# Kernel optimization log

Measured on AMD Instinct MI355X. Metric: run time of the kernel, lower is better.

## Reference

```python
import math
import jax, jax.numpy as jnp
import numpy as np

D = 2048
NH = 16
HD = D // NH
B_IMG = 32
H_ORIG, W_ORIG = 28, 36
POOL = 2
HF, WF = H_ORIG // POOL, W_ORIG // POOL  # 14, 18
T = HF * WF                              # 252 tokens per image
S_TOTAL = B_IMG * T                      # 8064
EPS = 1e-6


def setup_inputs() -> dict:
    key = jax.random.key(0)
    ks = jax.random.split(key, 12)
    w = lambda k, shp: jax.random.normal(k, shp, dtype=jnp.float32) * 0.02
    return {
        'semantic_hidden': jax.random.normal(ks[0], (1, S_TOTAL, D), jnp.float32),
        'vggt_features': jax.random.normal(ks[1], (1, S_TOTAL, D), jnp.float32),
        'grid_thw': jnp.tile(jnp.array([[1, H_ORIG, W_ORIG]], dtype=jnp.int64), (B_IMG, 1)),
        'ln1_w': jnp.ones((D,), jnp.float32), 'ln1_b': jnp.zeros((D,), jnp.float32),
        'ln2_w': jnp.ones((D,), jnp.float32), 'ln2_b': jnp.zeros((D,), jnp.float32),
        'Wq': w(ks[2], (D, D)), 'Wk': w(ks[3], (D, D)),
        'Wv': w(ks[4], (D, D)), 'Wo': w(ks[5], (D, D)),
        'imp_w1': w(ks[6], (D // 4, D)), 'imp_b1': jnp.zeros((D // 4,), jnp.float32),
        'imp_w2': w(ks[7], (1, D // 4)), 'imp_b2': jnp.zeros((1,), jnp.float32),
        'gate_w': w(ks[8], (NH // 2, D)), 'gate_b': jnp.zeros((NH // 2,), jnp.float32),
        'gate': jnp.asarray(0.5, jnp.float32),  # torch init is 0.0 (output would be all-zero); use 0.5 for a meaningful baseline
    }


def _layernorm(x, w, b):
    mu = jnp.mean(x, axis=-1, keepdims=True)
    var = jnp.var(x, axis=-1, keepdims=True)
    return (x - mu) * jax.lax.rsqrt(var + EPS) * w + b


def _spatial_bias(h_feat, w_feat, dtype):
    y = jnp.arange(h_feat, dtype=dtype)
    x = jnp.arange(w_feat, dtype=dtype)
    gy, gx = jnp.meshgrid(y, x, indexing='ij')
    coords = jnp.stack([gy.reshape(-1), gx.reshape(-1)], axis=-1)  # [N, 2]
    diff = coords[:, None, :] - coords[None, :, :]
    dist = jnp.sqrt(jnp.sum(diff * diff, axis=-1))  # [N, N]
    diag_len = math.sqrt(h_feat ** 2 + w_feat ** 2) + 1e-6
    return -dist / diag_len


def reference(semantic_hidden, vggt_features, grid_thw, ln1_w, ln1_b, ln2_w, ln2_b,
              Wq, Wk, Wv, Wo, imp_w1, imp_b1, imp_w2, imp_b2, gate_w, gate_b, gate):
    sem = _layernorm(semantic_hidden, ln1_w, ln1_b)
    vgg = _layernorm(vggt_features, ln2_w, ln2_b)
    B_orig, S_total, Dm = sem.shape

    # grid_thw is a static host constant -> Python ints (shapes must be static)
    h_feat = int(np.asarray(grid_thw)[0, 1]) // POOL
    w_feat = int(np.asarray(grid_thw)[0, 2]) // POOL
    tokens = h_feat * w_feat
    num_images = S_total // tokens

    q_in = sem.reshape(num_images, tokens, Dm)   # [B, S, D]
    kv_in = vgg.reshape(num_images, tokens, Dm)
    B, S = num_images, tokens

    q = (q_in @ Wq.T).reshape(B, S, NH, HD).transpose(0, 2, 1, 3)   # [B, H, S, hd]
    k = (kv_in @ Wk.T).reshape(B, S, NH, HD).transpose(0, 2, 1, 3)
    v = (kv_in @ Wv.T).reshape(B, S, NH, HD).transpose(0, 2, 1, 3)

    attn = jnp.einsum('bhqd,bhkd->bhqk', q, k) / math.sqrt(HD)       # [B, H, S, S]

    # spatial bias on first half of heads, gated per (image, query)
    sp_bias = _spatial_bias(h_feat, w_feat, q.dtype)                 # [S, S]
    gate_score = jax.nn.sigmoid(q_in @ gate_w.T + gate_b)            # [B, S, H/2]
    gate_score = gate_score.transpose(0, 2, 1)[..., None]            # [B, H/2, S, 1]
    split = NH // 2
    attn = attn.at[:, :split].add(sp_bias[None, None] * gate_score)

    # importance gate: log-importance bias over keys, shared across heads
    hidden = jax.nn.relu(q_in @ imp_w1.T + imp_b1)
    importance = jax.nn.sigmoid(hidden @ imp_w2.T + imp_b2)          # [B, S, 1]
    attn = attn + jnp.log(importance + 0.1).reshape(B, 1, 1, S)

    probs = jax.nn.softmax(attn, axis=-1)
    out = jnp.einsum('bhqk,bhkd->bhqd', probs, v)                    # [B, H, S, hd]
    out = out.transpose(0, 2, 1, 3).reshape(B, S, Dm)
    out = out.reshape(B_orig, S_total, Dm) @ Wo.T
    return jnp.tanh(gate) * out
```

## Files before the change

### kernel.cpp

```cpp
#include <hip/hip_runtime.h>
#include <hip/hip_bf16.h>
#include <math.h>

typedef __bf16 bf16_t;
typedef __bf16 bf16x8 __attribute__((ext_vector_type(8)));
typedef float f32x4v __attribute__((ext_vector_type(4)));
typedef unsigned short ushort_t;

#define SL_TOTAL 8064
#define DMODEL 2048
#define NHEAD 16
#define HDIM 128
#define SEQ 252

__device__ __forceinline__ bf16_t f2bf(float f) {
  unsigned u = __builtin_bit_cast(unsigned, f);
  u += 0x7fffu + ((u >> 16) & 1u);
  ushort_t h = (ushort_t)(u >> 16);
  return __builtin_bit_cast(bf16_t, h);
}
__device__ __forceinline__ float bf2f(bf16_t b) {
  unsigned u = ((unsigned)__builtin_bit_cast(ushort_t, b)) << 16;
  return __builtin_bit_cast(float, u);
}

__global__ __launch_bounds__(256) void cvt_kernel(const float* __restrict__ src,
                                                  bf16_t* __restrict__ dst, int n) {
  int i = (blockIdx.x * 256 + threadIdx.x) * 8;
  if (i >= n) return;
  float4 a = *(const float4*)(src + i);
  float4 b = *(const float4*)(src + i + 4);
  bf16x8 o;
  o[0] = f2bf(a.x); o[1] = f2bf(a.y); o[2] = f2bf(a.z); o[3] = f2bf(a.w);
  o[4] = f2bf(b.x); o[5] = f2bf(b.y); o[6] = f2bf(b.z); o[7] = f2bf(b.w);
  *(bf16x8*)(dst + i) = o;
}

__global__ __launch_bounds__(256) void ln_kernel(
    const float* __restrict__ sem, const float* __restrict__ vgg,
    const float* __restrict__ w1, const float* __restrict__ b1,
    const float* __restrict__ w2, const float* __restrict__ b2,
    bf16_t* __restrict__ o1, bf16_t* __restrict__ o2) {
  const float* x; const float* w; const float* bb; bf16_t* o;
  int row = blockIdx.x;
  if (blockIdx.y == 0) { x = sem; w = w1; bb = b1; o = o1; }
  else                 { x = vgg; w = w2; bb = b2; o = o2; }
  x += (size_t)row * DMODEL; o += (size_t)row * DMODEL;
  int t = threadIdx.x, wid = t >> 6, lane = t & 63;
  float4 va = *(const float4*)(x + t * 8);
  float4 vb = *(const float4*)(x + t * 8 + 4);
  float s  = va.x + va.y + va.z + va.w + vb.x + vb.y + vb.z + vb.w;
  float ss = va.x*va.x + va.y*va.y + va.z*va.z + va.w*va.w
           + vb.x*vb.x + vb.y*vb.y + vb.z*vb.z + vb.w*vb.w;
  #pragma unroll
  for (int m = 1; m < 64; m <<= 1) { s += __shfl_xor(s, m); ss += __shfl_xor(ss, m); }
  __shared__ float rs[4], rss[4];
  if (lane == 0) { rs[wid] = s; rss[wid] = ss; }
  __syncthreads();
  float st = rs[0] + rs[1] + rs[2] + rs[3];
  float sst = rss[0] + rss[1] + rss[2] + rss[3];
  float mu = st * (1.0f / 2048.0f);
  float var = sst * (1.0f / 2048.0f) - mu * mu;
  float rstd = rsqrtf(var + 1e-6f);
  float4 wa = *(const float4*)(w + t * 8);
  float4 wb = *(const float4*)(w + t * 8 + 4);
  float4 ba = *(const float4*)(bb + t * 8);
  float4 bb4 = *(const float4*)(bb + t * 8 + 4);
  bf16x8 ov;
  ov[0] = f2bf((va.x - mu) * rstd * wa.x + ba.x);
  ov[1] = f2bf((va.y - mu) * rstd * wa.y + ba.y);
  ov[2] = f2bf((va.z - mu) * rstd * wa.z + ba.z);
  ov[3] = f2bf((va.w - mu) * rstd * wa.w + ba.w);
  ov[4] = f2bf((vb.x - mu) * rstd * wb.x + bb4.x);
  ov[5] = f2bf((vb.y - mu) * rstd * wb.y + bb4.y);
  ov[6] = f2bf((vb.z - mu) * rstd * wb.z + bb4.z);
  ov[7] = f2bf((vb.w - mu) * rstd * wb.w + bb4.w);
  *(bf16x8*)(o + t * 8) = ov;
}

template <int EPI>
__global__ __launch_bounds__(256, 2) void gemm_bt(
    const bf16_t* __restrict__ A, const bf16_t* __restrict__ B,
    void* __restrict__ C, void* __restrict__ C2,
    const float* __restrict__ bias, const float* __restrict__ gatep,
    int M, int N, int K, int nnt) {
  __shared__ bf16_t As[2][128 * 64];
  __shared__ bf16_t Bs[2][128 * 64];
  const int nblk = gridDim.x;
  const int orig = blockIdx.x;
  const int qd = nblk >> 3, rr = nblk & 7, xc = orig & 7, lin = orig >> 3;
  const int wg = (xc < rr ? xc * (qd + 1) : rr * (qd + 1) + (xc - rr) * qd) + lin;
  const int mtile = wg / nnt;
  const int ntile = wg - mtile * nnt;
  const int m0 = mtile * 128, n0 = ntile * 128;

  const int tid = threadIdx.x;
  const int wid = tid >> 6, lane = tid & 63;
  const int l15 = lane & 15, l4 = lane >> 4;
  const int wm = (wid >> 1) * 64, wn = (wid & 1) * 64;
  const int srow = lane >> 3;
  const int scol = 8 * ((lane & 7) ^ (lane >> 3));

  f32x4v acc[4][4] = {};
  const int nkt = K >> 6;

  auto stage = [&](int kt, int buf) {
    const int k0 = kt << 6;
    #pragma unroll
    for (int it = 0; it < 4; ++it) {
      int chunk = wid + 4 * it;
      int row = chunk * 8 + srow;
      const bf16_t* ga = A + (size_t)(m0 + row) * K + k0 + scol;
      const bf16_t* gb = B + (size_t)(n0 + row) * K + k0 + scol;
      bf16_t* la = &As[buf][chunk * 512];
      bf16_t* lb = &Bs[buf][chunk * 512];
      __builtin_amdgcn_global_load_lds((const __attribute__((address_space(1))) unsigned int*)ga,
                                       (__attribute__((address_space(3))) unsigned int*)la, 16, 0, 0);
      __builtin_amdgcn_global_load_lds((const __attribute__((address_space(1))) unsigned int*)gb,
                                       (__attribute__((address_space(3))) unsigned int*)lb, 16, 0, 0);
    }
  };

  stage(0, 0);
  for (int kt = 0; kt < nkt; ++kt) {
    int buf = kt & 1;
    __syncthreads();
    if (kt + 1 < nkt) stage(kt + 1, buf ^ 1);
    const char* as = (const char*)As[buf];
    const char* bs = (const char*)Bs[buf];
    #pragma unroll
    for (int ki = 0; ki < 2; ++ki) {
      int cb = ki * 64 + l4 * 16;
      bf16x8 af[4], bfv[4];
      #pragma unroll
      for (int mi = 0; mi < 4; ++mi) {
        int row = wm + mi * 16 + l15;
        af[mi] = *(const bf16x8*)(as + row * 128 + (cb ^ ((row & 7) << 4)));
      }
      #pragma unroll
      for (int ni = 0; ni < 4; ++ni) {
        int row = wn + ni * 16 + l15;
        bfv[ni] = *(const bf16x8*)(bs + row * 128 + (cb ^ ((row & 7) << 4)));
      }
      #pragma unroll
      for (int mi = 0; mi < 4; ++mi)
        #pragma unroll
        for (int ni = 0; ni < 4; ++ni)
          acc[mi][ni] = __builtin_amdgcn_mfma_f32_16x16x32_bf16(af[mi], bfv[ni], acc[mi][ni], 0, 0, 0);
    }
    __syncthreads();
  }

  float scale = 1.0f;
  if (EPI == 2) scale = tanhf(gatep[0]);
  bf16_t* Cb = (bf16_t*)C;
  int colbase = n0;
  int ldc = N;
  if (EPI == 3) {
    ldc = 2048;
    if (n0 >= 2048) { Cb = (bf16_t*)C2; colbase = n0 - 2048; }
  }
  #pragma unroll
  for (int mi = 0; mi < 4; ++mi) {
    #pragma unroll
    for (int ni = 0; ni < 4; ++ni) {
      int c = colbase + wn + ni * 16 + l15;
      #pragma unroll
      for (int j = 0; j < 4; ++j) {
        int r = m0 + wm + mi * 16 + 4 * l4 + j;
        float v = acc[mi][ni][j];
        if (EPI == 1) { v += bias[c]; v = v > 0.0f ? v : 0.0f; }
        if (EPI == 2) ((float*)C)[(size_t)r * N + c] = v * scale;
        else Cb[(size_t)r * ldc + c] = f2bf(v);
      }
    }
  }
}

__global__ __launch_bounds__(256) void gate_kernel(const bf16_t* __restrict__ a,
                                                   const float* __restrict__ gw,
                                                   const float* __restrict__ gb,
                                                   float* __restrict__ gs) {
  int row = blockIdx.x;
  int t = threadIdx.x;
  int j = t >> 5, lt = t & 31;
  const bf16_t* ar = a + (size_t)row * DMODEL;
  const float* wr = gw + (size_t)j * DMODEL;
  float sum = 0.0f;
  #pragma unroll
  for (int u = 0; u < 8; ++u) {
    int i = lt * 8 + u * 256;
    bf16x8 av = *(const bf16x8*)(ar + i);
    float4 w0 = *(const float4*)(wr + i);
    float4 w1 = *(const float4*)(wr + i + 4);
    sum += bf2f(av[0]) * w0.x + bf2f(av[1]) * w0.y + bf2f(av[2]) * w0.z + bf2f(av[3]) * w0.w
         + bf2f(av[4]) * w1.x + bf2f(av[5]) * w1.y + bf2f(av[6]) * w1.z + bf2f(av[7]) * w1.w;
  }
  #pragma unroll
  for (int m = 1; m < 32; m <<= 1) sum += __shfl_xor(sum, m);
  if (lt == 0) gs[(size_t)row * 8 + j] = 1.0f / (1.0f + __expf(-(sum + gb[j])));
}

__global__ __launch_bounds__(256) void imp_kernel(const bf16_t* __restrict__ hid,
                                                  const float* __restrict__ w2,
                                                  const float* __restrict__ b2,
                                                  float* __restrict__ kb) {
  int row = blockIdx.x * 4 + (threadIdx.x >> 6);
  int lane = threadIdx.x & 63;
  const bf16_t* hr = hid + (size_t)row * 512;
  bf16x8 hv = *(const bf16x8*)(hr + lane * 8);
  float sum = 0.0f;
  #pragma unroll
  for (int i = 0; i < 8; ++i) sum += bf2f(hv[i]) * w2[lane * 8 + i];
  #pragma unroll
  for (int m = 1; m < 64; m <<= 1) sum += __shfl_xor(sum, m);
  if (lane == 0) {
    float imp = 1.0f / (1.0f + __expf(-(sum + b2[0])));
    kb[row] = logf(imp + 0.1f);
  }
}

__global__ __launch_bounds__(512, 1) void attn_kernel(
    const bf16_t* __restrict__ Q, const bf16_t* __restrict__ K,
    const bf16_t* __restrict__ V, const float* __restrict__ gs,
    const float* __restrict__ kb, bf16_t* __restrict__ O) {
  __shared__ bf16_t Kt[64 * 128];
  __shared__ bf16_t Vt[128 * 64];
  __shared__ bf16_t Pl[8][32 * 72];
  __shared__ float kyf[256], kxf[256], kbl[256];

  const int bi = blockIdx.x >> 4;
  const int h = blockIdx.x & 15;
  const int tid = threadIdx.x;
  const int wid = tid >> 6;
  const int lane = tid & 63;
  const int l15 = lane & 15, l4 = lane >> 4;
  const bool hs = (h < 8);

  for (int i = tid; i < 256; i += 512) {
    kyf[i] = (float)(i / 18);
    kxf[i] = (float)(i % 18);
    int kk = i < SEQ ? i : SEQ - 1;
    kbl[i] = kb[bi * SEQ + kk];
  }

  const int q0 = wid * 32;
  bf16x8 qf[2][4];
  #pragma unroll
  for (int mi = 0; mi < 2; ++mi) {
    int q = q0 + mi * 16 + l15; if (q >= SEQ) q = SEQ - 1;
    const bf16_t* qp = Q + (size_t)(bi * SEQ + q) * DMODEL + h * HDIM;
    #pragma unroll
    for (int ki = 0; ki < 4; ++ki) qf[mi][ki] = *(const bf16x8*)(qp + ki * 32 + l4 * 8);
  }

  float gsv[2][4], qyv[2][4], qxv[2][4];
  #pragma unroll
  for (int mi = 0; mi < 2; ++mi)
    #pragma unroll
    for (int j = 0; j < 4; ++j) {
      int q = q0 + mi * 16 + 4 * l4 + j;
      int qc = q < SEQ ? q : SEQ - 1;
      gsv[mi][j] = hs ? gs[(size_t)(bi * SEQ + qc) * 8 + h] : 0.0f;
      qyv[mi][j] = (float)(q / 18);
      qxv[mi][j] = (float)(q % 18);
    }

  float mrow[2][4], lrow[2][4];
  #pragma unroll
  for (int mi = 0; mi < 2; ++mi)
    #pragma unroll
    for (int j = 0; j < 4; ++j) { mrow[mi][j] = -3.0e38f; lrow[mi][j] = 0.0f; }

  f32x4v oacc[2][8] = {};
  const float scl = 0.08838834764831845f;
  const float invdiag = 1.0f / (sqrtf(520.0f) + 1e-6f);
  bf16_t* Plw = &Pl[wid][0];

  for (int t = 0; t < 4; ++t) {
    __syncthreads();
    #pragma unroll
    for (int rep = 0; rep < 2; ++rep) {
      int s = tid + rep * 512;
      int row = s >> 4, cb = s & 15;
      int kk = t * 64 + row;
      uint4 val = make_uint4(0, 0, 0, 0);
      if (kk < SEQ) val = *(const uint4*)(K + (size_t)(bi * SEQ + kk) * DMODEL + h * HDIM + cb * 8);
      *(uint4*)((char*)Kt + row * 256 + ((cb * 16) ^ ((row & 7) << 4))) = val;
    }
    {
      int kp = tid >> 4, db = tid & 15;
      int k0i = t * 64 + kp * 2, k1i = k0i + 1;
      uint4 a = make_uint4(0, 0, 0, 0), c4 = make_uint4(0, 0, 0, 0);
      if (k0i < SEQ) a = *(const uint4*)(V + (size_t)(bi * SEQ + k0i) * DMODEL + h * HDIM + db * 8);
      if (k1i < SEQ) c4 = *(const uint4*)(V + (size_t)(bi * SEQ + k1i) * DMODEL + h * HDIM + db * 8);
      const ushort_t* au = (const ushort_t*)&a;
      const ushort_t* cu = (const ushort_t*)&c4;
      #pragma unroll
      for (int i = 0; i < 8; ++i) {
        int d = db * 8 + i;
        unsigned pv = (unsigned)au[i] | ((unsigned)cu[i] << 16);
        *(unsigned*)((char*)Vt + d * 128 + ((kp * 4) ^ ((d & 7) << 4))) = pv;
      }
    }
    __syncthreads();

    f32x4v sc[2][4] = {};
    #pragma unroll
    for (int ki = 0; ki < 4; ++ki) {
      bf16x8 kf[4];
      #pragma unroll
      for (int ni = 0; ni < 4; ++ni) {
        int row = ni * 16 + l15;
        kf[ni] = *(const bf16x8*)((char*)Kt + row * 256 + ((ki * 64 + l4 * 16) ^ ((row & 7) << 4)));
      }
      #pragma unroll
      for (int mi = 0; mi < 2; ++mi)
        #pragma unroll
        for (int ni = 0; ni < 4; ++ni)
          sc[mi][ni] = __builtin_amdgcn_mfma_f32_16x16x32_bf16(qf[mi][ki], kf[ni], sc[mi][ni], 0, 0, 0);
    }

    #pragma unroll
    for (int mi = 0; mi < 2; ++mi) {
      #pragma unroll
      for (int j = 0; j < 4; ++j) {
        float s4[4];
        float rm = -3.0e38f;
        #pragma unroll
        for (int ni = 0; ni < 4; ++ni) {
          int kk = t * 64 + ni * 16 + l15;
          float s = sc[mi][ni][j] * scl + kbl[kk];
          if (hs) {
            float dy = qyv[mi][j] - kyf[kk];
            float dx = qxv[mi][j] - kxf[kk];
            s -= sqrtf(dy * dy + dx * dx) * invdiag * gsv[mi][j];
          }
          if (kk >= SEQ) s = -3.0e38f;
          s4[ni] = s;
          rm = fmaxf(rm, s);
        }
        #pragma unroll
        for (int msk = 1; msk < 16; msk <<= 1) rm = fmaxf(rm, __shfl_xor(rm, msk));
        float mold = mrow[mi][j];
        float mnew = fmaxf(mold, rm);
        float corr = __expf(mold - mnew);
        float rsum = 0.0f;
        #pragma unroll
        for (int ni = 0; ni < 4; ++ni) {
          float p = __expf(s4[ni] - mnew);
          s4[ni] = p;
          rsum += p;
        }
        #pragma unroll
        for (int msk = 1; msk < 16; msk <<= 1) rsum += __shfl_xor(rsum, msk);
        mrow[mi][j] = mnew;
        lrow[mi][j] = lrow[mi][j] * corr + rsum;
        #pragma unroll
        for (int di = 0; di < 8; ++di) oacc[mi][di][j] *= corr;
        int prow = mi * 16 + 4 * l4 + j;
        #pragma unroll
        for (int ni = 0; ni < 4; ++ni)
          Plw[prow * 72 + ni * 16 + l15] = f2bf(s4[ni]);
      }
    }

    #pragma unroll
    for (int ks = 0; ks < 2; ++ks) {
      bf16x8 pf[2];
      #pragma unroll
      for (int mi = 0; mi < 2; ++mi)
        pf[mi] = *(const bf16x8*)(Plw + (mi * 16 + l15) * 72 + ks * 32 + l4 * 8);
      #pragma unroll
      for (int di = 0; di < 8; ++di) {
        int d = di * 16 + l15;
        bf16x8 vf = *(const bf16x8*)((char*)Vt + d * 128 + ((ks * 64 + l4 * 16) ^ ((d & 7) << 4)));
        #pragma unroll
        for (int mi = 0; mi < 2; ++mi)
          oacc[mi][di] = __builtin_amdgcn_mfma_f32_16x16x32_bf16(pf[mi], vf, oacc[mi][di], 0, 0, 0);
      }
    }
  }

  #pragma unroll
  for (int mi = 0; mi < 2; ++mi) {
    #pragma unroll
    for (int j = 0; j < 4; ++j) {
      int q = q0 + mi * 16 + 4 * l4 + j;
      if (q >= SEQ) continue;
      float inv = 1.0f / lrow[mi][j];
      bf16_t* op = O + (size_t)(bi * SEQ + q) * DMODEL + h * HDIM;
      #pragma unroll
      for (int di = 0; di < 8; ++di)
        op[di * 16 + l15] = f2bf(oacc[mi][di][j] * inv);
    }
  }
}

extern "C" void kernel_launch(void* const* d_in, const int* in_sizes, int n_in,
                              void* d_out, int out_size, void* d_ws, size_t ws_size,
                              hipStream_t stream) {
  const float* sem  = (const float*)d_in[0];
  const float* vgg  = (const float*)d_in[1];
  const float* ln1w = (const float*)d_in[3];
  const float* ln1b = (const float*)d_in[4];
  const float* ln2w = (const float*)d_in[5];
  const float* ln2b = (const float*)d_in[6];
  const float* Wq   = (const float*)d_in[7];
  const float* Wk   = (const float*)d_in[8];
  const float* Wv   = (const float*)d_in[9];
  const float* Wo   = (const float*)d_in[10];
  const float* w1   = (const float*)d_in[11];
  const float* b1   = (const float*)d_in[12];
  const float* w2   = (const float*)d_in[13];
  const float* b2   = (const float*)d_in[14];
  const float* gw   = (const float*)d_in[15];
  const float* gb   = (const float*)d_in[16];
  const float* gate = (const float*)d_in[17];

  char* ws = (char*)d_ws;
  const size_t SZ_W = 8388608;
  const size_t SZ_ACT = 33030144;
  bf16_t* Wqb  = (bf16_t*)(ws + 0);
  bf16_t* Wkb  = (bf16_t*)(ws + SZ_W);
  bf16_t* Wvb  = (bf16_t*)(ws + 2 * SZ_W);
  bf16_t* Wob  = (bf16_t*)(ws + 3 * SZ_W);
  bf16_t* w1b  = (bf16_t*)(ws + 4 * SZ_W);
  bf16_t* semb = (bf16_t*)(ws + 4 * SZ_W + 2097152);
  bf16_t* vggb = (bf16_t*)(ws + 4 * SZ_W + 2097152 + SZ_ACT);
  bf16_t* Vb   = (bf16_t*)(ws + 4 * SZ_W + 2097152 + 2 * SZ_ACT);
  bf16_t* hidb = (bf16_t*)(ws + 4 * SZ_W + 2097152 + 3 * SZ_ACT);
  float*  gsb  = (float*)(ws + 4 * SZ_W + 2097152 + 3 * SZ_ACT + 8257536);
  float*  kbb  = (float*)(ws + 4 * SZ_W + 2097152 + 3 * SZ_ACT + 8257536 + 258048);
  bf16_t* Qb = (bf16_t*)d_out;
  bf16_t* Kb = (bf16_t*)((char*)d_out + SZ_ACT);
  bf16_t* attnb = semb;

  cvt_kernel<<<2048, 256, 0, stream>>>(Wq, Wqb, 4194304);
  cvt_kernel<<<2048, 256, 0, stream>>>(Wk, Wkb, 4194304);
  cvt_kernel<<<2048, 256, 0, stream>>>(Wv, Wvb, 4194304);
  cvt_kernel<<<2048, 256, 0, stream>>>(Wo, Wob, 4194304);
  cvt_kernel<<<512, 256, 0, stream>>>(w1, w1b, 1048576);
  ln_kernel<<<dim3(8064, 2), 256, 0, stream>>>(sem, vgg, ln1w, ln1b, ln2w, ln2b, semb, vggb);

  gemm_bt<0><<<1008, 256, 0, stream>>>(semb, Wqb, Qb, nullptr, nullptr, nullptr,
                                       8064, 2048, 2048, 16);
  gemm_bt<3><<<2016, 256, 0, stream>>>(vggb, Wkb, Kb, Vb, nullptr, nullptr,
                                       8064, 4096, 2048, 32);
  gemm_bt<1><<<252, 256, 0, stream>>>(semb, w1b, hidb, nullptr, b1, nullptr,
                                      8064, 512, 2048, 4);

  gate_kernel<<<8064, 256, 0, stream>>>(semb, gw, gb, gsb);
  imp_kernel<<<2016, 256, 0, stream>>>(hidb, w2, b2, kbb);

  attn_kernel<<<512, 512, 0, stream>>>(Qb, Kb, Vb, gsb, kbb, attnb);

  gemm_bt<2><<<1008, 256, 0, stream>>>(attnb, Wob, d_out, nullptr, nullptr, gate,
                                       8064, 2048, 2048, 16);
}
```

Before: 532.9 us.

## Use 256x128 GEMM tiles with triple-buffered LDS pipeline and 8 waves

Replaces the 128x128 double-buffered GEMM with a 256x128 tile kernel using 512 threads, a three-stage global-to-LDS pipeline with explicit vmcnt waits and a single barrier per k-step, and raised wave priority around the MFMA block. M is padded to 8192 so the last tile reads padding rows, with stores masked by the real row count, and workspace buffers are re-laid out with padded activation slots. The aim is to cut barrier and load-latency stalls and raise data reuse per tile, at the cost of one block per CU, more LDS, and some wasted compute on padded rows.

```diff
diff --git a/kernel.cpp b/kernel.cpp
--- a/kernel.cpp
+++ b/kernel.cpp
@@ -8,6 +8,7 @@
 typedef unsigned short ushort_t;
 
 #define SL_TOTAL 8064
+#define SL_PAD 8192
 #define DMODEL 2048
 #define NHEAD 16
 #define HDIM 128
@@ -79,76 +80,92 @@
 }
 
 template <int EPI>
-__global__ __launch_bounds__(256, 2) void gemm_bt(
+__global__ __launch_bounds__(512, 1) void gemm3(
     const bf16_t* __restrict__ A, const bf16_t* __restrict__ B,
     void* __restrict__ C, void* __restrict__ C2,
     const float* __restrict__ bias, const float* __restrict__ gatep,
-    int M, int N, int K, int nnt) {
-  __shared__ bf16_t As[2][128 * 64];
-  __shared__ bf16_t Bs[2][128 * 64];
+    int Mreal, int N, int K, int nnt) {
+  __shared__ bf16_t As[3][256 * 64];
+  __shared__ bf16_t Bs[3][128 * 64];
   const int nblk = gridDim.x;
   const int orig = blockIdx.x;
   const int qd = nblk >> 3, rr = nblk & 7, xc = orig & 7, lin = orig >> 3;
   const int wg = (xc < rr ? xc * (qd + 1) : rr * (qd + 1) + (xc - rr) * qd) + lin;
   const int mtile = wg / nnt;
   const int ntile = wg - mtile * nnt;
-  const int m0 = mtile * 128, n0 = ntile * 128;
+  const int m0 = mtile * 256, n0 = ntile * 128;
 
   const int tid = threadIdx.x;
   const int wid = tid >> 6, lane = tid & 63;
   const int l15 = lane & 15, l4 = lane >> 4;
   const int wm = (wid >> 1) * 64, wn = (wid & 1) * 64;
   const int srow = lane >> 3;
-  const int scol = 8 * ((lane & 7) ^ (lane >> 3));
+  const int scol = 8 * ((lane & 7) ^ srow);
 
   f32x4v acc[4][4] = {};
-  const int nkt = K >> 6;
-
-  auto stage = [&](int kt, int buf) {
+  const int NKT = K >> 6;
+
+  auto stage = [&](int kt) {
+    const int buf = kt % 3;
     const int k0 = kt << 6;
     #pragma unroll
     for (int it = 0; it < 4; ++it) {
-      int chunk = wid + 4 * it;
+      int chunk = wid + 8 * it;
       int row = chunk * 8 + srow;
       const bf16_t* ga = A + (size_t)(m0 + row) * K + k0 + scol;
+      __builtin_amdgcn_global_load_lds((const __attribute__((address_space(1))) unsigned int*)ga,
+                                       (__attribute__((address_space(3))) unsigned int*)&As[buf][chunk * 512],
+                                       16, 0, 0);
+    }
+    #pragma unroll
+    for (int it = 0; it < 2; ++it) {
+      int chunk = wid + 8 * it;
+      int row = chunk * 8 + srow;
       const bf16_t* gb = B + (size_t)(n0 + row) * K + k0 + scol;
-      bf16_t* la = &As[buf][chunk * 512];
-      bf16_t* lb = &Bs[buf][chunk * 512];
-      __builtin_amdgcn_global_load_lds((const __attribute__((address_space(1))) unsigned int*)ga,
-                                       (__attribute__((address_space(3))) unsigned int*)la, 16, 0, 0);
       __builtin_amdgcn_global_load_lds((const __attribute__((address_space(1))) unsigned int*)gb,
-                                       (__attribute__((address_space(3))) unsigned int*)lb, 16, 0, 0);
+                                       (__attribute__((address_space(3))) unsigned int*)&Bs[buf][chunk * 512],
+                                       16, 0, 0);
     }
   };
 
-  stage(0, 0);
-  for (int kt = 0; kt < nkt; ++kt) {
-    int buf = kt & 1;
-    __syncthreads();
-    if (kt + 1 < nkt) stage(kt + 1, buf ^ 1);
-    const char* as = (const char*)As[buf];
-    const char* bs = (const char*)Bs[buf];
-    #pragma unroll
-    for (int ki = 0; ki < 2; ++ki) {
-      int cb = ki * 64 + l4 * 16;
-      bf16x8 af[4], bfv[4];
+  stage(0);
+  stage(1);
+
+  for (int kt = 0; kt < NKT; ++kt) {
+    const int cb3 = kt % 3;
+    if (kt < NKT - 1) asm volatile("s_waitcnt vmcnt(6)" ::: "memory");
+    else              asm volatile("s_waitcnt vmcnt(0)" ::: "memory");
+    __builtin_amdgcn_s_barrier();
+    __builtin_amdgcn_sched_barrier(0);
+    if (kt + 2 < NKT) stage(kt + 2);
+    const char* as = (const char*)As[cb3];
+    const char* bs = (const char*)Bs[cb3];
+    bf16x8 af[2][4], bfv[2][4];
+    #pragma unroll
+    for (int ks = 0; ks < 2; ++ks) {
+      int cb = ks * 64 + l4 * 16;
       #pragma unroll
       for (int mi = 0; mi < 4; ++mi) {
         int row = wm + mi * 16 + l15;
-        af[mi] = *(const bf16x8*)(as + row * 128 + (cb ^ ((row & 7) << 4)));
+        af[ks][mi] = *(const bf16x8*)(as + row * 128 + (cb ^ ((row & 7) << 4)));
       }
       #pragma unroll
       for (int ni = 0; ni < 4; ++ni) {
         int row = wn + ni * 16 + l15;
-        bfv[ni] = *(const bf16x8*)(bs + row * 128 + (cb ^ ((row & 7) << 4)));
-      }
+        bfv[ks][ni] = *(const bf16x8*)(bs + row * 128 + (cb ^ ((row & 7) << 4)));
+      }
+    }
+    asm volatile("s_waitcnt lgkmcnt(0)" ::: "memory");
+    __builtin_amdgcn_sched_barrier(0);
+    __builtin_amdgcn_s_setprio(1);
+    #pragma unroll
+    for (int ks = 0; ks < 2; ++ks)
       #pragma unroll
       for (int mi = 0; mi < 4; ++mi)
         #pragma unroll
         for (int ni = 0; ni < 4; ++ni)
-          acc[mi][ni] = __builtin_amdgcn_mfma_f32_16x16x32_bf16(af[mi], bfv[ni], acc[mi][ni], 0, 0, 0);
-    }
-    __syncthreads();
+          acc[mi][ni] = __builtin_amdgcn_mfma_f32_16x16x32_bf16(af[ks][mi], bfv[ks][ni], acc[mi][ni], 0, 0, 0);
+    __builtin_amdgcn_s_setprio(0);
   }
 
   float scale = 1.0f;
@@ -168,6 +185,7 @@
       #pragma unroll
       for (int j = 0; j < 4; ++j) {
         int r = m0 + wm + mi * 16 + 4 * l4 + j;
+        if (r >= Mreal) continue;
         float v = acc[mi][ni][j];
         if (EPI == 1) { v += bias[c]; v = v > 0.0f ? v : 0.0f; }
         if (EPI == 2) ((float*)C)[(size_t)r * N + c] = v * scale;
@@ -419,19 +437,20 @@
   const float* gate = (const float*)d_in[17];
 
   char* ws = (char*)d_ws;
-  const size_t SZ_W = 8388608;
-  const size_t SZ_ACT = 33030144;
+  const size_t SZ_W    = 8388608;
+  const size_t SZ_PAD  = 33554432;
+  const size_t SZ_ACT  = 33030144;
   bf16_t* Wqb  = (bf16_t*)(ws + 0);
   bf16_t* Wkb  = (bf16_t*)(ws + SZ_W);
   bf16_t* Wvb  = (bf16_t*)(ws + 2 * SZ_W);
   bf16_t* Wob  = (bf16_t*)(ws + 3 * SZ_W);
   bf16_t* w1b  = (bf16_t*)(ws + 4 * SZ_W);
   bf16_t* semb = (bf16_t*)(ws + 4 * SZ_W + 2097152);
-  bf16_t* vggb = (bf16_t*)(ws + 4 * SZ_W + 2097152 + SZ_ACT);
-  bf16_t* Vb   = (bf16_t*)(ws + 4 * SZ_W + 2097152 + 2 * SZ_ACT);
-  bf16_t* hidb = (bf16_t*)(ws + 4 * SZ_W + 2097152 + 3 * SZ_ACT);
-  float*  gsb  = (float*)(ws + 4 * SZ_W + 2097152 + 3 * SZ_ACT + 8257536);
-  float*  kbb  = (float*)(ws + 4 * SZ_W + 2097152 + 3 * SZ_ACT + 8257536 + 258048);
+  bf16_t* vggb = (bf16_t*)(ws + 4 * SZ_W + 2097152 + SZ_PAD);
+  bf16_t* Vb   = (bf16_t*)(ws + 4 * SZ_W + 2097152 + 2 * SZ_PAD);
+  bf16_t* hidb = (bf16_t*)(ws + 4 * SZ_W + 2097152 + 2 * SZ_PAD + SZ_ACT);
+  float*  gsb  = (float*)(ws + 4 * SZ_W + 2097152 + 2 * SZ_PAD + SZ_ACT + 8257536);
+  float*  kbb  = (float*)(ws + 4 * SZ_W + 2097152 + 2 * SZ_PAD + SZ_ACT + 8257536 + 258048);
   bf16_t* Qb = (bf16_t*)d_out;
   bf16_t* Kb = (bf16_t*)((char*)d_out + SZ_ACT);
   bf16_t* attnb = semb;
@@ -443,18 +462,18 @@
   cvt_kernel<<<512, 256, 0, stream>>>(w1, w1b, 1048576);
   ln_kernel<<<dim3(8064, 2), 256, 0, stream>>>(sem, vgg, ln1w, ln1b, ln2w, ln2b, semb, vggb);
 
-  gemm_bt<0><<<1008, 256, 0, stream>>>(semb, Wqb, Qb, nullptr, nullptr, nullptr,
-                                       8064, 2048, 2048, 16);
-  gemm_bt<3><<<2016, 256, 0, stream>>>(vggb, Wkb, Kb, Vb, nullptr, nullptr,
-                                       8064, 4096, 2048, 32);
-  gemm_bt<1><<<252, 256, 0, stream>>>(semb, w1b, hidb, nullptr, b1, nullptr,
-                                      8064, 512, 2048, 4);
+  gemm3<0><<<512, 512, 0, stream>>>(semb, Wqb, Qb, nullptr, nullptr, nullptr,
+                                    8064, 2048, 2048, 16);
+  gemm3<3><<<1024, 512, 0, stream>>>(vggb, Wkb, Kb, Vb, nullptr, nullptr,
+                                     8064, 4096, 2048, 32);
+  gemm3<1><<<128, 512, 0, stream>>>(semb, w1b, hidb, nullptr, b1, nullptr,
+                                    8064, 512, 2048, 4);
 
   gate_kernel<<<8064, 256, 0, stream>>>(semb, gw, gb, gsb);
   imp_kernel<<<2016, 256, 0, stream>>>(hidb, w2, b2, kbb);
 
   attn_kernel<<<512, 512, 0, stream>>>(Qb, Kb, Vb, gsb, kbb, attnb);
 
-  gemm_bt<2><<<1008, 256, 0, stream>>>(attnb, Wob, d_out, nullptr, nullptr, gate,
-                                       8064, 2048, 2048, 16);
-}
+  gemm3<2><<<512, 512, 0, stream>>>(attnb, Wob, d_out, nullptr, nullptr, gate,
+                                    8064, 2048, 2048, 16);
+}
```

Result: slower. 599.5 us (+12.5%).

## Use 256x256 ping-pong GEMM for Q/KV/O projections, batch conversions and gate rows

Applied to the files above, without the earlier changes.

Adds a 512-thread GEMM kernel with 256x256 tiles, direct global-to-LDS loads, priority-controlled interleaving and masked tail rows. It replaces the 128x128 GEMM for the Q, fused K/V and output projections to raise operand reuse and MFMA density. The activation buffers are padded to 8192 rows so the last tile can read past 8064 rows without faulting. It also merges the four weight conversions into one launch and makes the gate kernel compute four rows per block. The cost is larger LDS use per block and fewer blocks, which may leave some CUs idle.

```diff
diff --git a/kernel.cpp b/kernel.cpp
--- a/kernel.cpp
+++ b/kernel.cpp
@@ -8,6 +8,7 @@
 typedef unsigned short ushort_t;
 
 #define SL_TOTAL 8064
+#define SL_PAD 8192
 #define DMODEL 2048
 #define NHEAD 16
 #define HDIM 128
@@ -22,6 +23,30 @@
 __device__ __forceinline__ float bf2f(bf16_t b) {
   unsigned u = ((unsigned)__builtin_bit_cast(ushort_t, b)) << 16;
   return __builtin_bit_cast(float, u);
+}
+
+__global__ __launch_bounds__(256) void cvt4_kernel(const float* __restrict__ s0,
+                                                   const float* __restrict__ s1,
+                                                   const float* __restrict__ s2,
+                                                   const float* __restrict__ s3,
+                                                   bf16_t* __restrict__ d0,
+                                                   bf16_t* __restrict__ d1,
+                                                   bf16_t* __restrict__ d2,
+                                                   bf16_t* __restrict__ d3) {
+  const float* src; bf16_t* dst;
+  switch (blockIdx.y) {
+    case 0: src = s0; dst = d0; break;
+    case 1: src = s1; dst = d1; break;
+    case 2: src = s2; dst = d2; break;
+    default: src = s3; dst = d3; break;
+  }
+  int i = (blockIdx.x * 256 + threadIdx.x) * 8;
+  float4 a = *(const float4*)(src + i);
+  float4 b = *(const float4*)(src + i + 4);
+  bf16x8 o;
+  o[0] = f2bf(a.x); o[1] = f2bf(a.y); o[2] = f2bf(a.z); o[3] = f2bf(a.w);
+  o[4] = f2bf(b.x); o[5] = f2bf(b.y); o[6] = f2bf(b.z); o[7] = f2bf(b.w);
+  *(bf16x8*)(dst + i) = o;
 }
 
 __global__ __launch_bounds__(256) void cvt_kernel(const float* __restrict__ src,
@@ -79,6 +104,165 @@
 }
 
 template <int EPI>
+__global__ __launch_bounds__(512, 2) void gemm256(
+    const bf16_t* __restrict__ A, const bf16_t* __restrict__ B,
+    void* __restrict__ C, void* __restrict__ C2,
+    const float* __restrict__ gatep,
+    int Mreal, int N, int K, int nnt) {
+  __shared__ bf16_t As[2][256 * 64];
+  __shared__ bf16_t Bs[2][256 * 64];
+  const int nblk = gridDim.x;
+  const int orig = blockIdx.x;
+  const int qd = nblk >> 3, rr = nblk & 7, xc = orig & 7, lin = orig >> 3;
+  const int wg = (xc < rr ? xc * (qd + 1) : rr * (qd + 1) + (xc - rr) * qd) + lin;
+  const int mtile = wg / nnt, ntile = wg - mtile * nnt;
+  const int m0 = mtile * 256, n0 = ntile * 256;
+
+  const int tid = threadIdx.x;
+  const int wid = tid >> 6, lane = tid & 63;
+  const int l15 = lane & 15, l4 = lane >> 4;
+  const int wr = wid >> 2, wc = wid & 3;
+  const int srow = lane >> 3;
+  const int scol = 8 * ((lane & 7) ^ srow);
+
+  f32x4v acc[8][4] = {};
+  const int NKT = K >> 6;
+
+  auto stage_all = [&](int kt, bf16_t* an, bf16_t* bn) {
+    const int k0 = kt << 6;
+    #pragma unroll
+    for (int it = 0; it < 4; ++it) {
+      int chunk = wid + 8 * it;
+      int row = chunk * 8 + srow;
+      const bf16_t* ga = A + (size_t)(m0 + row) * K + k0 + scol;
+      __builtin_amdgcn_global_load_lds((const __attribute__((address_space(1))) unsigned int*)ga,
+          (__attribute__((address_space(3))) unsigned int*)(an + chunk * 512), 16, 0, 0);
+    }
+    #pragma unroll
+    for (int it = 0; it < 4; ++it) {
+      int chunk = wid + 8 * it;
+      int row = chunk * 8 + srow;
+      const bf16_t* gb = B + (size_t)(n0 + row) * K + k0 + scol;
+      __builtin_amdgcn_global_load_lds((const __attribute__((address_space(1))) unsigned int*)gb,
+          (__attribute__((address_space(3))) unsigned int*)(bn + chunk * 512), 16, 0, 0);
+    }
+  };
+
+  auto ld_a = [&](const bf16_t* as, int ks, int mi) -> bf16x8 {
+    int row = wr * 128 + mi * 16 + l15;
+    int cb = ks * 64 + l4 * 16;
+    return *(const bf16x8*)((const char*)as + row * 128 + (cb ^ ((row & 7) << 4)));
+  };
+  auto ld_b = [&](const bf16_t* bs, int ks, int ni) -> bf16x8 {
+    int row = wc * 64 + ni * 16 + l15;
+    int cb = ks * 64 + l4 * 16;
+    return *(const bf16x8*)((const char*)bs + row * 128 + (cb ^ ((row & 7) << 4)));
+  };
+
+  auto tile_step = [&](int t, const bf16_t* as, const bf16_t* bs,
+                       bf16_t* an, bf16_t* bn) {
+    bf16x8 af[4], bfv[4];
+    #pragma unroll
+    for (int mi = 0; mi < 4; ++mi) af[mi] = ld_a(as, 0, mi);
+    #pragma unroll
+    for (int ni = 0; ni < 4; ++ni) bfv[ni] = ld_b(bs, 0, ni);
+    if (t + 1 < NKT) stage_all(t + 1, an, bn);
+    __builtin_amdgcn_s_barrier();
+    asm volatile("s_waitcnt lgkmcnt(0)" ::: "memory");
+    __builtin_amdgcn_sched_barrier(0);
+    __builtin_amdgcn_s_setprio(1);
+    #pragma unroll
+    for (int mi = 0; mi < 4; ++mi)
+      #pragma unroll
+      for (int ni = 0; ni < 4; ++ni)
+        acc[mi][ni] = __builtin_amdgcn_mfma_f32_16x16x32_bf16(af[mi], bfv[ni], acc[mi][ni], 0, 0, 0);
+    __builtin_amdgcn_s_setprio(0);
+    __builtin_amdgcn_s_barrier();
+    __builtin_amdgcn_sched_barrier(0);
+    #pragma unroll
+    for (int mi = 0; mi < 4; ++mi) af[mi] = ld_a(as, 0, mi + 4);
+    __builtin_amdgcn_s_barrier();
+    asm volatile("s_waitcnt lgkmcnt(0)" ::: "memory");
+    __builtin_amdgcn_sched_barrier(0);
+    __builtin_amdgcn_s_setprio(1);
+    #pragma unroll
+    for (int mi = 0; mi < 4; ++mi)
+      #pragma unroll
+      for (int ni = 0; ni < 4; ++ni)
+        acc[mi + 4][ni] = __builtin_amdgcn_mfma_f32_16x16x32_bf16(af[mi], bfv[ni], acc[mi + 4][ni], 0, 0, 0);
+    __builtin_amdgcn_s_setprio(0);
+    __builtin_amdgcn_s_barrier();
+    __builtin_amdgcn_sched_barrier(0);
+    #pragma unroll
+    for (int mi = 0; mi < 4; ++mi) af[mi] = ld_a(as, 1, mi);
+    #pragma unroll
+    for (int ni = 0; ni < 4; ++ni) bfv[ni] = ld_b(bs, 1, ni);
+    __builtin_amdgcn_s_barrier();
+    asm volatile("s_waitcnt lgkmcnt(0)" ::: "memory");
+    __builtin_amdgcn_sched_barrier(0);
+    __builtin_amdgcn_s_setprio(1);
+    #pragma unroll
+    for (int mi = 0; mi < 4; ++mi)
+      #pragma unroll
+      for (int ni = 0; ni < 4; ++ni)
+        acc[mi][ni] = __builtin_amdgcn_mfma_f32_16x16x32_bf16(af[mi], bfv[ni], acc[mi][ni], 0, 0, 0);
+    __builtin_amdgcn_s_setprio(0);
+    __builtin_amdgcn_s_barrier();
+    __builtin_amdgcn_sched_barrier(0);
+    #pragma unroll
+    for (int mi = 0; mi < 4; ++mi) af[mi] = ld_a(as, 1, mi + 4);
+    __builtin_amdgcn_s_barrier();
+    asm volatile("s_waitcnt lgkmcnt(0)" ::: "memory");
+    __builtin_amdgcn_sched_barrier(0);
+    __builtin_amdgcn_s_setprio(1);
+    #pragma unroll
+    for (int mi = 0; mi < 4; ++mi)
+      #pragma unroll
+      for (int ni = 0; ni < 4; ++ni)
+        acc[mi + 4][ni] = __builtin_amdgcn_mfma_f32_16x16x32_bf16(af[mi], bfv[ni], acc[mi + 4][ni], 0, 0, 0);
+    __builtin_amdgcn_s_setprio(0);
+    if (t + 1 < NKT) asm volatile("s_waitcnt vmcnt(0)" ::: "memory");
+    __builtin_amdgcn_s_barrier();
+    __builtin_amdgcn_sched_barrier(0);
+  };
+
+  stage_all(0, As[0], Bs[0]);
+  asm volatile("s_waitcnt vmcnt(0)" ::: "memory");
+  __builtin_amdgcn_s_barrier();
+  __builtin_amdgcn_sched_barrier(0);
+
+  for (int t = 0; t < NKT; t += 2) {
+    tile_step(t,     As[0], Bs[0], As[1], Bs[1]);
+    tile_step(t + 1, As[1], Bs[1], As[0], Bs[0]);
+  }
+
+  float scale = 1.0f;
+  if (EPI == 2) scale = tanhf(gatep[0]);
+  bf16_t* Cb = (bf16_t*)C;
+  int colbase = n0;
+  int ldc = N;
+  if (EPI == 3) {
+    ldc = 2048;
+    if (n0 >= 2048) { Cb = (bf16_t*)C2; colbase = n0 - 2048; }
+  }
+  #pragma unroll
+  for (int mi = 0; mi < 8; ++mi) {
+    #pragma unroll
+    for (int ni = 0; ni < 4; ++ni) {
+      int c = colbase + wc * 64 + ni * 16 + l15;
+      #pragma unroll
+      for (int j = 0; j < 4; ++j) {
+        int r = m0 + wr * 128 + mi * 16 + 4 * l4 + j;
+        if (r >= Mreal) continue;
+        float v = acc[mi][ni][j];
+        if (EPI == 2) ((float*)C)[(size_t)r * N + c] = v * scale;
+        else Cb[(size_t)r * ldc + c] = f2bf(v);
+      }
+    }
+  }
+}
+
+template <int EPI>
 __global__ __launch_bounds__(256, 2) void gemm_bt(
     const bf16_t* __restrict__ A, const bf16_t* __restrict__ B,
     void* __restrict__ C, void* __restrict__ C2,
@@ -151,27 +335,17 @@
     __syncthreads();
   }
 
-  float scale = 1.0f;
-  if (EPI == 2) scale = tanhf(gatep[0]);
-  bf16_t* Cb = (bf16_t*)C;
-  int colbase = n0;
-  int ldc = N;
-  if (EPI == 3) {
-    ldc = 2048;
-    if (n0 >= 2048) { Cb = (bf16_t*)C2; colbase = n0 - 2048; }
-  }
   #pragma unroll
   for (int mi = 0; mi < 4; ++mi) {
     #pragma unroll
     for (int ni = 0; ni < 4; ++ni) {
-      int c = colbase + wn + ni * 16 + l15;
+      int c = n0 + wn + ni * 16 + l15;
       #pragma unroll
       for (int j = 0; j < 4; ++j) {
         int r = m0 + wm + mi * 16 + 4 * l4 + j;
         float v = acc[mi][ni][j];
         if (EPI == 1) { v += bias[c]; v = v > 0.0f ? v : 0.0f; }
-        if (EPI == 2) ((float*)C)[(size_t)r * N + c] = v * scale;
-        else Cb[(size_t)r * ldc + c] = f2bf(v);
+        ((bf16_t*)C)[(size_t)r * N + c] = f2bf(v);
       }
     }
   }
@@ -181,24 +355,33 @@
                                                    const float* __restrict__ gw,
                                                    const float* __restrict__ gb,
                                                    float* __restrict__ gs) {
-  int row = blockIdx.x;
+  int r0 = blockIdx.x * 4;
   int t = threadIdx.x;
   int j = t >> 5, lt = t & 31;
-  const bf16_t* ar = a + (size_t)row * DMODEL;
   const float* wr = gw + (size_t)j * DMODEL;
-  float sum = 0.0f;
+  float sum[4] = {0.0f, 0.0f, 0.0f, 0.0f};
   #pragma unroll
   for (int u = 0; u < 8; ++u) {
     int i = lt * 8 + u * 256;
-    bf16x8 av = *(const bf16x8*)(ar + i);
     float4 w0 = *(const float4*)(wr + i);
     float4 w1 = *(const float4*)(wr + i + 4);
-    sum += bf2f(av[0]) * w0.x + bf2f(av[1]) * w0.y + bf2f(av[2]) * w0.z + bf2f(av[3]) * w0.w
-         + bf2f(av[4]) * w1.x + bf2f(av[5]) * w1.y + bf2f(av[6]) * w1.z + bf2f(av[7]) * w1.w;
-  }
-  #pragma unroll
-  for (int m = 1; m < 32; m <<= 1) sum += __shfl_xor(sum, m);
-  if (lt == 0) gs[(size_t)row * 8 + j] = 1.0f / (1.0f + __expf(-(sum + gb[j])));
+    #pragma unroll
+    for (int r = 0; r < 4; ++r) {
+      bf16x8 av = *(const bf16x8*)(a + (size_t)(r0 + r) * DMODEL + i);
+      sum[r] += bf2f(av[0]) * w0.x + bf2f(av[1]) * w0.y + bf2f(av[2]) * w0.z + bf2f(av[3]) * w0.w
+              + bf2f(av[4]) * w1.x + bf2f(av[5]) * w1.y + bf2f(av[6]) * w1.z + bf2f(av[7]) * w1.w;
+    }
+  }
+  #pragma unroll
+  for (int m = 1; m < 32; m <<= 1) {
+    #pragma unroll
+    for (int r = 0; r < 4; ++r) sum[r] += __shfl_xor(sum[r], m);
+  }
+  if (lt == 0) {
+    #pragma unroll
+    for (int r = 0; r < 4; ++r)
+      gs[(size_t)(r0 + r) * 8 + j] = 1.0f / (1.0f + __expf(-(sum[r] + gb[j])));
+  }
 }
 
 __global__ __launch_bounds__(256) void imp_kernel(const bf16_t* __restrict__ hid,
@@ -419,42 +602,40 @@
   const float* gate = (const float*)d_in[17];
 
   char* ws = (char*)d_ws;
-  const size_t SZ_W = 8388608;
-  const size_t SZ_ACT = 33030144;
+  const size_t SZ_W    = 8388608;
+  const size_t SZ_PAD  = 33554432;
+  const size_t SZ_ACT  = 33030144;
   bf16_t* Wqb  = (bf16_t*)(ws + 0);
   bf16_t* Wkb  = (bf16_t*)(ws + SZ_W);
   bf16_t* Wvb  = (bf16_t*)(ws + 2 * SZ_W);
   bf16_t* Wob  = (bf16_t*)(ws + 3 * SZ_W);
   bf16_t* w1b  = (bf16_t*)(ws + 4 * SZ_W);
   bf16_t* semb = (bf16_t*)(ws + 4 * SZ_W + 2097152);
-  bf16_t* vggb = (bf16_t*)(ws + 4 * SZ_W + 2097152 + SZ_ACT);
-  bf16_t* Vb   = (bf16_t*)(ws + 4 * SZ_W + 2097152 + 2 * SZ_ACT);
-  bf16_t* hidb = (bf16_t*)(ws + 4 * SZ_W + 2097152 + 3 * SZ_ACT);
-  float*  gsb  = (float*)(ws + 4 * SZ_W + 2097152 + 3 * SZ_ACT + 8257536);
-  float*  kbb  = (float*)(ws + 4 * SZ_W + 2097152 + 3 * SZ_ACT + 8257536 + 258048);
+  bf16_t* vggb = (bf16_t*)(ws + 4 * SZ_W + 2097152 + SZ_PAD);
+  bf16_t* Vb   = (bf16_t*)(ws + 4 * SZ_W + 2097152 + 2 * SZ_PAD);
+  bf16_t* hidb = (bf16_t*)(ws + 4 * SZ_W + 2097152 + 2 * SZ_PAD + SZ_ACT);
+  float*  gsb  = (float*)(ws + 4 * SZ_W + 2097152 + 2 * SZ_PAD + SZ_ACT + 8257536);
+  float*  kbb  = (float*)(ws + 4 * SZ_W + 2097152 + 2 * SZ_PAD + SZ_ACT + 8257536 + 258048);
   bf16_t* Qb = (bf16_t*)d_out;
   bf16_t* Kb = (bf16_t*)((char*)d_out + SZ_ACT);
   bf16_t* attnb = semb;
 
-  cvt_kernel<<<2048, 256, 0, stream>>>(Wq, Wqb, 4194304);
-  cvt_kernel<<<2048, 256, 0, stream>>>(Wk, Wkb, 4194304);
-  cvt_kernel<<<2048, 256, 0, stream>>>(Wv, Wvb, 4194304);
-  cvt_kernel<<<2048, 256, 0, stream>>>(Wo, Wob, 4194304);
+  cvt4_kernel<<<dim3(2048, 4), 256, 0, stream>>>(Wq, Wk, Wv, Wo, Wqb, Wkb, Wvb, Wob);
   cvt_kernel<<<512, 256, 0, stream>>>(w1, w1b, 1048576);
   ln_kernel<<<dim3(8064, 2), 256, 0, stream>>>(sem, vgg, ln1w, ln1b, ln2w, ln2b, semb, vggb);
 
-  gemm_bt<0><<<1008, 256, 0, stream>>>(semb, Wqb, Qb, nullptr, nullptr, nullptr,
-                                       8064, 2048, 2048, 16);
-  gemm_bt<3><<<2016, 256, 0, stream>>>(vggb, Wkb, Kb, Vb, nullptr, nullptr,
-                                       8064, 4096, 2048, 32);
+  gemm256<0><<<256, 512, 0, stream>>>(semb, Wqb, Qb, nullptr, nullptr,
+                                      8064, 2048, 2048, 8);
+  gemm256<3><<<512, 512, 0, stream>>>(vggb, Wkb, Kb, Vb, nullptr,
+                                      8064, 4096, 2048, 16);
   gemm_bt<1><<<252, 256, 0, stream>>>(semb, w1b, hidb, nullptr, b1, nullptr,
                                       8064, 512, 2048, 4);
 
-  gate_kernel<<<8064, 256, 0, stream>>>(semb, gw, gb, gsb);
+  gate_kernel<<<2016, 256, 0, stream>>>(semb, gw, gb, gsb);
   imp_kernel<<<2016, 256, 0, stream>>>(hidb, w2, b2, kbb);
 
   attn_kernel<<<512, 512, 0, stream>>>(Qb, Kb, Vb, gsb, kbb, attnb);
 
-  gemm_bt<2><<<1008, 256, 0, stream>>>(attnb, Wob, d_out, nullptr, nullptr, gate,
-                                       8064, 2048, 2048, 16);
-}
+  gemm256<2><<<256, 512, 0, stream>>>(attnb, Wob, d_out, nullptr, gate,
+                                      8064, 2048, 2048, 8);
+}
```

After: 500.3 us. -6.1%, faster.
